# Kernel optimization log

Hardware: AMD Instinct MI355X
Metric: run time of the kernel (lower is better)

The kernel has to match this reference:

```python
import jax, jax.numpy as jnp
import numpy as np

B, C, H, W = 4, 192, 256, 256
P = 8          # patch_size; d_model = P, input_size = P*P
R = 4          # FFN expansion ratio
SLOPE = 0.01   # torch default leaky_relu negative_slope


def _conv(x, w, pad):
    return jax.lax.conv_general_dilated(x, w, (1, 1), pad,
                                        dimension_numbers=('NCHW', 'OIHW', 'NCHW'))


def setup_inputs() -> dict:
    key = jax.random.key(0)
    ks = jax.random.split(key, 16)
    p2 = P * P
    s = 0.05
    return {
        'x':  jax.random.normal(ks[0], (B, C, H, W), jnp.float32),
        # per-window linear attention params (torch Linear stored as (in,out))
        'Wq': jax.random.normal(ks[1], (p2, P), jnp.float32) * s,
        'bq': jnp.zeros((P,), jnp.float32),
        'Wk': jax.random.normal(ks[2], (p2, P), jnp.float32) * s,
        'bk': jnp.zeros((P,), jnp.float32),
        'Wv': jax.random.normal(ks[3], (p2, P), jnp.float32) * s,
        'bv': jnp.zeros((P,), jnp.float32),
        'Wo': jax.random.normal(ks[4], (P, p2), jnp.float32) * s,
        'bo': jnp.zeros((p2,), jnp.float32),
        # FFN conv params
        'W1': jax.random.normal(ks[5], (C * R, C, 1, 1), jnp.float32) * s,
        'b1': jnp.zeros((C * R,), jnp.float32),
        'W2': jax.random.normal(ks[6], (C * R, C * R, 3, 3), jnp.float32) * s,
        'b2': jnp.zeros((C * R,), jnp.float32),
        'W3': jax.random.normal(ks[7], (C, C * R, 1, 1), jnp.float32) * s,
        'b3': jnp.zeros((C,), jnp.float32),
    }


def reference(x, Wq, bq, Wk, bk, Wv, bv, Wo, bo, W1, b1, W2, b2, W3, b3):
    Bb, Cc, Hh, Ww = x.shape
    nh, nw = Hh // P, Ww // P
    N = nh * nw
    # crop patches: (B, N, C, P*P), window-major row order (i over rows, j over cols)
    xp = (x.reshape(Bb, Cc, nh, P, nw, P)
           .transpose(0, 2, 4, 1, 3, 5)
           .reshape(Bb, N, Cc, P * P))
    # softplus-kernel linear attention over the CHANNEL axis (weight is CxC per window)
    q = jax.nn.softplus(xp @ Wq + bq)            # (B,N,C,P)
    k = jax.nn.softplus(xp @ Wk + bk)            # (B,N,C,P)
    v = xp @ Wv + bv                              # (B,N,C,P)
    w = jnp.einsum('bncd,bnhd->bnch', q, k)      # (B,N,C,C)
    r = jnp.einsum('bnch,bnhd->bncd', w, v)      # (B,N,C,P)
    attn = r @ Wo + bo                            # (B,N,C,P*P)
    y = xp + attn                                 # in-place residual in the original
    # Merge_patches: cat along height then reshape == contiguous reinterpret
    feat = (y.reshape(Bb, N, Cc, P, P)
             .transpose(0, 2, 1, 3, 4)
             .reshape(Bb, Cc, nh * P, nw * P))
    h = jax.nn.leaky_relu(_conv(feat, W1, 'VALID') + b1[:, None, None], SLOPE)
    h = jax.nn.leaky_relu(_conv(h, W2, 'SAME') + b2[:, None, None], SLOPE)
    out = jax.nn.leaky_relu(_conv(h, W3, 'VALID') + b3[:, None, None], SLOPE)
    return out
```

## Files before the change

kernel.cpp:

```cpp
#include <hip/hip_runtime.h>
#include <stdint.h>
#include <math.h>

typedef _Float16 half_t;
typedef _Float16 f16x8 __attribute__((ext_vector_type(8)));
typedef float f32x4 __attribute__((ext_vector_type(4)));

#define SLOPE 0.01f

__device__ inline float leaky(float v) { return v > 0.f ? v : SLOPE * v; }

__device__ inline void stage16(const half_t* g, half_t* l) {
    __builtin_amdgcn_global_load_lds(
        (const __attribute__((address_space(1))) unsigned int*)g,
        (__attribute__((address_space(3))) unsigned int*)l, 16, 0, 0);
}

__device__ inline float softplusf(float v) {
    return v > 20.f ? v : log1pf(expf(v));
}

__global__ void prep_kernel(const float* __restrict__ W1, const float* __restrict__ W2,
                            const float* __restrict__ W3,
                            half_t* __restrict__ B1w, half_t* __restrict__ B2w,
                            half_t* __restrict__ B3w)
{
    const unsigned idx = blockIdx.x * 256u + threadIdx.x;
    const unsigned n2 = 768u * 6912u;
    if (idx < n2) {
        unsigned oc = idx / 6912u;
        unsigned rem = idx - oc * 6912u;
        unsigned tap = rem / 768u;
        unsigned ic = rem - tap * 768u;
        unsigned ky = tap / 3u, kx = tap - ky * 3u;
        B2w[idx] = (half_t)W2[(((size_t)oc * 768u + ic) * 3u + ky) * 3u + kx];
    } else if (idx < n2 + 147456u) {
        unsigned i = idx - n2;
        B1w[i] = (half_t)W1[i];
    } else if (idx < n2 + 294912u) {
        unsigned i = idx - n2 - 147456u;
        B3w[i] = (half_t)W3[i];
    }
}

__global__ __launch_bounds__(256, 2)
void attn_kernel(const float* __restrict__ x,
                 const float* __restrict__ Wq, const float* __restrict__ bq,
                 const float* __restrict__ Wk, const float* __restrict__ bk,
                 const float* __restrict__ Wv, const float* __restrict__ bv,
                 const float* __restrict__ Wo, const float* __restrict__ bo,
                 half_t* __restrict__ featN)
{
    __shared__ half_t xls[192 * 65];
    __shared__ float wqL[512], wkL[512], wvL[512], woL[512];
    __shared__ float bqL[8], bkL[8], bvL[8], boL[64];
    __shared__ float kls[192 * 9], vls[192 * 9];
    __shared__ float sls[64];

    const int t = threadIdx.x;
    const int blk = blockIdx.x;
    const int b = blk >> 10;
    const int n = blk & 1023;
    const int wi = n >> 5, wj = n & 31;

    for (int i = t; i < 512; i += 256) {
        wqL[i] = Wq[i]; wkL[i] = Wk[i]; wvL[i] = Wv[i]; woL[i] = Wo[i];
    }
    if (t < 8)  { bqL[t] = bq[t]; bkL[t] = bk[t]; bvL[t] = bv[t]; }
    if (t < 64) boL[t] = bo[t];

    #pragma unroll
    for (int i = 0; i < 6; ++i) {
        int idx = t + i * 256;
        int c = idx >> 3, py = idx & 7;
        const float* src = x + (((size_t)b * 192 + c) * 256 + (wi * 8 + py)) * 256 + wj * 8;
        float4 v0 = *(const float4*)src;
        float4 v1 = *(const float4*)(src + 4);
        half_t* dst = &xls[c * 65 + py * 8];
        dst[0] = (half_t)v0.x; dst[1] = (half_t)v0.y; dst[2] = (half_t)v0.z; dst[3] = (half_t)v0.w;
        dst[4] = (half_t)v1.x; dst[5] = (half_t)v1.y; dst[6] = (half_t)v1.z; dst[7] = (half_t)v1.w;
    }
    __syncthreads();

    float qf[8], kf[8], vf[8];
    if (t < 192) {
        #pragma unroll
        for (int d = 0; d < 8; ++d) { qf[d] = bqL[d]; kf[d] = bkL[d]; vf[d] = bvL[d]; }
        const half_t* xr = &xls[t * 65];
        for (int p = 0; p < 64; ++p) {
            float xv = (float)xr[p];
            const float* wqp = &wqL[p * 8];
            const float* wkp = &wkL[p * 8];
            const float* wvp = &wvL[p * 8];
            #pragma unroll
            for (int d = 0; d < 8; ++d) {
                qf[d] += xv * wqp[d];
                kf[d] += xv * wkp[d];
                vf[d] += xv * wvp[d];
            }
        }
        #pragma unroll
        for (int d = 0; d < 8; ++d) {
            qf[d] = softplusf(qf[d]);
            kf[d] = softplusf(kf[d]);
            kls[t * 9 + d] = kf[d];
            vls[t * 9 + d] = vf[d];
        }
    }
    __syncthreads();
    if (t < 64) {
        int e = t >> 3, dd = t & 7;
        float s = 0.f;
        for (int c = 0; c < 192; ++c) s += kls[c * 9 + e] * vls[c * 9 + dd];
        sls[t] = s;
    }
    __syncthreads();
    if (t < 192) {
        float rf[8];
        #pragma unroll
        for (int d = 0; d < 8; ++d) {
            float s = 0.f;
            #pragma unroll
            for (int e = 0; e < 8; ++e) s += qf[e] * sls[e * 8 + d];
            rf[d] = s;
        }
        half_t* xr = &xls[t * 65];
        for (int p = 0; p < 64; ++p) {
            float a = boL[p];
            #pragma unroll
            for (int d = 0; d < 8; ++d) a += rf[d] * woL[d * 64 + p];
            xr[p] = (half_t)((float)xr[p] + a);
        }
    }
    __syncthreads();
    half_t* dst = featN + ((size_t)b * 65536 + (size_t)n * 64) * 192;
    for (int i = 0; i < 48; ++i) {
        int idx = t + i * 256;
        int p = idx / 192, c = idx - p * 192;
        dst[idx] = xls[c * 65 + p];
    }
}

__global__ __launch_bounds__(256, 2)
void conv1_kernel(const half_t* __restrict__ featN, const half_t* __restrict__ B1w,
                  const float* __restrict__ b1, half_t* __restrict__ h1p, int batch)
{
    __shared__ half_t As[128 * 64];
    __shared__ half_t Bs[128 * 64];
    const int t = threadIdx.x;
    const int lane = t & 63;
    const int w = t >> 6;
    const int m0 = blockIdx.x * 128;
    const int n0 = blockIdx.y * 128;
    const int wm = (w >> 1) * 64, wn = (w & 1) * 64;
    const int rbase = t >> 3;
    const int g = (t & 7) ^ (rbase & 7);
    const int ar = lane & 15, kc = lane >> 4;

    f32x4 acc[4][4];
    #pragma unroll
    for (int i = 0; i < 4; ++i)
        #pragma unroll
        for (int j = 0; j < 4; ++j) acc[i][j] = (f32x4){0.f, 0.f, 0.f, 0.f};

    const size_t mb = (size_t)batch * 65536 + m0;

    for (int s = 0; s < 3; ++s) {
        const int k0 = s * 64;
        const half_t* ga = featN + (mb + rbase) * 192 + k0 + g * 8;
        const half_t* gb = B1w + (size_t)(n0 + rbase) * 192 + k0 + g * 8;
        half_t* la = As + t * 8;
        half_t* lb = Bs + t * 8;
        #pragma unroll
        for (int i = 0; i < 4; ++i) {
            stage16(ga + (size_t)32 * i * 192, la + 2048 * i);
            stage16(gb + (size_t)32 * i * 192, lb + 2048 * i);
        }
        __syncthreads();
        #pragma unroll
        for (int kh = 0; kh < 2; ++kh) {
            f16x8 af[4], bfr[4];
            const int c = kh * 4 + kc;
            #pragma unroll
            for (int mf = 0; mf < 4; ++mf) {
                int r = wm + mf * 16 + ar;
                af[mf] = *(const f16x8*)&As[(r * 8 + (c ^ (r & 7))) * 8];
            }
            #pragma unroll
            for (int nf = 0; nf < 4; ++nf) {
                int r = wn + nf * 16 + ar;
                bfr[nf] = *(const f16x8*)&Bs[(r * 8 + (c ^ (r & 7))) * 8];
            }
            #pragma unroll
            for (int mf = 0; mf < 4; ++mf)
                #pragma unroll
                for (int nf = 0; nf < 4; ++nf)
                    acc[mf][nf] = __builtin_amdgcn_mfma_f32_16x16x32_f16(af[mf], bfr[nf], acc[mf][nf], 0, 0, 0);
        }
        __syncthreads();
    }

    const int y = m0 >> 8, x0 = m0 & 255;
    half_t* outrow = h1p + ((size_t)(y + 1) * 258 + (x0 + 1)) * 768;
    #pragma unroll
    for (int nf = 0; nf < 4; ++nf) {
        int n = n0 + wn + nf * 16 + ar;
        float bias = b1[n];
        #pragma unroll
        for (int mf = 0; mf < 4; ++mf) {
            #pragma unroll
            for (int r4 = 0; r4 < 4; ++r4) {
                int local = wm + mf * 16 + kc * 4 + r4;
                outrow[(size_t)local * 768 + n] = (half_t)leaky(acc[mf][nf][r4] + bias);
            }
        }
    }
}

__device__ __forceinline__ void c2_stage_A(half_t* As, int buf, int h,
    const half_t* __restrict__ h1p, int y, int kstep, int t, int cg)
{
    const int tap = kstep / 12, icc = kstep - tap * 12;
    const int ky = tap / 3, kx = tap - ky * 3;
    const int row0 = t >> 3;
    const half_t* g = h1p + ((size_t)(y + ky) * 258 + (kx + h * 128 + row0)) * 768
                      + icc * 64 + cg;
    half_t* l = As + (buf * 2 + h) * 8192 + t * 8;
    stage16(g, l);
    stage16(g + (size_t)64 * 768, l + 4096);
}

__device__ __forceinline__ void c2_stage_B(half_t* Bs, int buf, int h,
    const half_t* __restrict__ B2w, int n0, int kstep, int t, int cg)
{
    const int tap = kstep / 12, icc = kstep - tap * 12;
    const int row0 = t >> 3;
    const half_t* g = B2w + (size_t)(n0 + h * 128 + row0) * 6912
                      + tap * 768 + icc * 64 + cg;
    half_t* l = Bs + (buf * 2 + h) * 8192 + t * 8;
    stage16(g, l);
    stage16(g + (size_t)64 * 6912, l + 4096);
}

#define SBAR __builtin_amdgcn_s_barrier()
#define SB0  __builtin_amdgcn_sched_barrier(0)
#define LGKM(N) asm volatile("s_waitcnt lgkmcnt(" #N ")" ::: "memory")
#define VMC(N)  asm volatile("s_waitcnt vmcnt(" #N ")" ::: "memory")

#define RDA(MQ, BUF)                                                             \
  _Pragma("unroll")                                                              \
  for (int mf = 0; mf < 4; ++mf)                                                 \
    _Pragma("unroll")                                                            \
    for (int kh = 0; kh < 2; ++kh) {                                             \
      const int lr = wm * 64 + mf * 16 + ar;                                     \
      const int ch = (kh * 4 + kc) ^ (lr & 7);                                   \
      af[MQ][mf][kh] = *(const f16x8*)&As[((BUF)*2 + (MQ))*8192 + lr*64 + ch*8]; \
    }

#define RDB(NQ, BUF)                                                             \
  _Pragma("unroll")                                                              \
  for (int nf = 0; nf < 2; ++nf)                                                 \
    _Pragma("unroll")                                                            \
    for (int kh = 0; kh < 2; ++kh) {                                             \
      const int lc = wn * 32 + nf * 16 + ar;                                     \
      const int ch = (kh * 4 + kc) ^ (lc & 7);                                   \
      bf[NQ][nf][kh] = *(const f16x8*)&Bs[((BUF)*2 + (NQ))*8192 + lc*64 + ch*8]; \
    }

#define MMA16(MQ, NQ)                                                            \
  {                                                                              \
    __builtin_amdgcn_s_setprio(1);                                               \
    _Pragma("unroll")                                                            \
    for (int kh = 0; kh < 2; ++kh)                                               \
      _Pragma("unroll")                                                          \
      for (int mf = 0; mf < 4; ++mf)                                             \
        _Pragma("unroll")                                                        \
        for (int nf = 0; nf < 2; ++nf)                                           \
          acc[(MQ)*2+(NQ)][mf][nf] = __builtin_amdgcn_mfma_f32_16x16x32_f16(     \
              af[MQ][mf][kh], bf[NQ][nf][kh], acc[(MQ)*2+(NQ)][mf][nf], 0, 0, 0);\
    __builtin_amdgcn_s_setprio(0);                                               \
  }

__global__ __launch_bounds__(512, 2)
void conv2_kernel(const half_t* __restrict__ h1p, const half_t* __restrict__ B2w,
                  const float* __restrict__ b2, half_t* __restrict__ h2)
{
    __shared__ half_t As[4 * 8192];
    __shared__ half_t Bs[4 * 8192];

    const int t = threadIdx.x;
    const int lane = t & 63;
    const int w = t >> 6;
    const int wm = w >> 2, wn = w & 3;
    const int ar = lane & 15, kc = lane >> 4;
    const int cg = (((t & 7) ^ ((t >> 3) & 7)) << 3);

    const int bid = blockIdx.x;
    const int xcd = bid & 7, sid = bid >> 3;
    const int wg = xcd * 96 + sid;
    const int mtile = wg / 3;
    const int nt = wg - mtile * 3;
    const int y = mtile;
    const int m0 = mtile * 256;
    const int n0 = nt * 256;

    f32x4 acc[4][4][2];
    #pragma unroll
    for (int q = 0; q < 4; ++q)
        #pragma unroll
        for (int i = 0; i < 4; ++i)
            #pragma unroll
            for (int j = 0; j < 2; ++j) acc[q][i][j] = (f32x4){0.f, 0.f, 0.f, 0.f};

    f16x8 af[2][4][2];
    f16x8 bf[2][2][2];

    c2_stage_A(As, 0, 0, h1p, y, 0, t, cg);
    c2_stage_A(As, 0, 1, h1p, y, 0, t, cg);
    c2_stage_B(Bs, 0, 0, B2w, n0, 0, t, cg);
    c2_stage_B(Bs, 0, 1, B2w, n0, 0, t, cg);
    c2_stage_A(As, 1, 0, h1p, y, 1, t, cg);
    c2_stage_A(As, 1, 1, h1p, y, 1, t, cg);
    c2_stage_B(Bs, 1, 0, B2w, n0, 1, t, cg);
    c2_stage_B(Bs, 1, 1, B2w, n0, 1, t, cg);
    VMC(0);
    SBAR; SB0;
    RDB(0, 0); SB0;
    RDA(0, 0);

    for (int i = 0; i < 53; ++i) {
        const int k2 = 2 * i + 2;
        const int k3 = 2 * i + 3;
        RDB(1, 0); SB0;
        RDA(1, 0);
        LGKM(12); SB0;
        MMA16(0, 0);
        SBAR;
        c2_stage_A(As, 0, 0, h1p, y, k2, t, cg);
        c2_stage_B(Bs, 0, 0, B2w, n0, k2, t, cg);
        LGKM(8); SB0;
        MMA16(0, 1);
        SBAR;
        LGKM(0); SB0;
        MMA16(1, 1);
        SBAR;
        c2_stage_A(As, 0, 1, h1p, y, k2, t, cg);
        c2_stage_B(Bs, 0, 1, B2w, n0, k2, t, cg);
        VMC(8);
        SBAR; SB0;
        MMA16(1, 0);
        SB0;
        RDB(0, 1); SB0;
        RDA(0, 1);
        SBAR;
        RDB(1, 1); SB0;
        RDA(1, 1);
        LGKM(12); SB0;
        MMA16(0, 0);
        SBAR;
        c2_stage_A(As, 1, 0, h1p, y, k3, t, cg);
        c2_stage_B(Bs, 1, 0, B2w, n0, k3, t, cg);
        LGKM(8); SB0;
        MMA16(0, 1);
        SBAR;
        LGKM(0); SB0;
        MMA16(1, 1);
        SBAR;
        c2_stage_A(As, 1, 1, h1p, y, k3, t, cg);
        c2_stage_B(Bs, 1, 1, B2w, n0, k3, t, cg);
        VMC(8);
        SBAR; SB0;
        MMA16(1, 0);
        SB0;
        RDB(0, 0); SB0;
        RDA(0, 0);
        SBAR;
    }
    {
        RDB(1, 0); SB0;
        RDA(1, 0);
        LGKM(12); SB0;
        MMA16(0, 0);
        SBAR;
        LGKM(8); SB0;
        MMA16(0, 1);
        SBAR;
        LGKM(0); SB0;
        MMA16(1, 1);
        SBAR;
        VMC(0);
        SBAR; SB0;
        MMA16(1, 0);
        SB0;
        RDB(0, 1); SB0;
        RDA(0, 1);
        SBAR;
        RDB(1, 1); SB0;
        RDA(1, 1);
        LGKM(12); SB0;
        MMA16(0, 0);
        SBAR;
        LGKM(8); SB0;
        MMA16(0, 1);
        SBAR;
        LGKM(0); SB0;
        MMA16(1, 1);
        SBAR;
        MMA16(1, 0);
    }

    #pragma unroll
    for (int q = 0; q < 4; ++q) {
        const int mq = q >> 1, nq = q & 1;
        #pragma unroll
        for (int nf = 0; nf < 2; ++nf) {
            const int col = n0 + nq * 128 + wn * 32 + nf * 16 + ar;
            const float bias = b2[col];
            #pragma unroll
            for (int mf = 0; mf < 4; ++mf) {
                const int row = m0 + mq * 128 + wm * 64 + mf * 16 + kc * 4;
                half_t* op = h2 + (size_t)row * 768 + col;
                #pragma unroll
                for (int r4 = 0; r4 < 4; ++r4)
                    op[(size_t)r4 * 768] = (half_t)leaky(acc[q][mf][nf][r4] + bias);
            }
        }
    }
}

__global__ __launch_bounds__(256, 2)
void conv3_kernel(const half_t* __restrict__ h2, const half_t* __restrict__ B3w,
                  const float* __restrict__ b3, float* __restrict__ out, int batch)
{
    __shared__ half_t As[128 * 64];
    __shared__ half_t Bs[192 * 64];
    const int t = threadIdx.x;
    const int lane = t & 63;
    const int w = t >> 6;
    const int m0 = blockIdx.x * 128;
    const int wm = (w >> 1) * 64;
    const int wn = (w & 1) * 96;
    const int rbase = t >> 3;
    const int g = (t & 7) ^ (rbase & 7);
    const int ar = lane & 15, kc = lane >> 4;

    f32x4 acc[4][6];
    #pragma unroll
    for (int i = 0; i < 4; ++i)
        #pragma unroll
        for (int j = 0; j < 6; ++j) acc[i][j] = (f32x4){0.f, 0.f, 0.f, 0.f};

    for (int s = 0; s < 12; ++s) {
        const int k0 = s * 64;
        const half_t* ga = h2 + (size_t)(m0 + rbase) * 768 + k0 + g * 8;
        const half_t* gb = B3w + (size_t)rbase * 768 + k0 + g * 8;
        half_t* la = As + t * 8;
        half_t* lb = Bs + t * 8;
        #pragma unroll
        for (int i = 0; i < 4; ++i) stage16(ga + (size_t)32 * i * 768, la + 2048 * i);
        #pragma unroll
        for (int i = 0; i < 6; ++i) stage16(gb + (size_t)32 * i * 768, lb + 2048 * i);
        __syncthreads();
        #pragma unroll
        for (int kh = 0; kh < 2; ++kh) {
            f16x8 af[4], bfr[6];
            const int c = kh * 4 + kc;
            #pragma unroll
            for (int mf = 0; mf < 4; ++mf) {
                int r = wm + mf * 16 + ar;
                af[mf] = *(const f16x8*)&As[(r * 8 + (c ^ (r & 7))) * 8];
            }
            #pragma unroll
            for (int nf = 0; nf < 6; ++nf) {
                int r = wn + nf * 16 + ar;
                bfr[nf] = *(const f16x8*)&Bs[(r * 8 + (c ^ (r & 7))) * 8];
            }
            #pragma unroll
            for (int mf = 0; mf < 4; ++mf)
                #pragma unroll
                for (int nf = 0; nf < 6; ++nf)
                    acc[mf][nf] = __builtin_amdgcn_mfma_f32_16x16x32_f16(af[mf], bfr[nf], acc[mf][nf], 0, 0, 0);
        }
        __syncthreads();
    }

    #pragma unroll
    for (int nf = 0; nf < 6; ++nf) {
        int n = wn + nf * 16 + ar;
        float bias = b3[n];
        float* op = out + ((size_t)batch * 192 + n) * 65536 + m0;
        #pragma unroll
        for (int mf = 0; mf < 4; ++mf) {
            int local = wm + mf * 16 + kc * 4;
            f32x4 v;
            #pragma unroll
            for (int r4 = 0; r4 < 4; ++r4) v[r4] = leaky(acc[mf][nf][r4] + bias);
            *(f32x4*)(op + local) = v;
        }
    }
}

extern "C" void kernel_launch(void* const* d_in, const int* in_sizes, int n_in,
                              void* d_out, int out_size, void* d_ws, size_t ws_size,
                              hipStream_t stream)
{
    const float* x  = (const float*)d_in[0];
    const float* Wq = (const float*)d_in[1];
    const float* bq = (const float*)d_in[2];
    const float* Wk = (const float*)d_in[3];
    const float* bk = (const float*)d_in[4];
    const float* Wv = (const float*)d_in[5];
    const float* bv = (const float*)d_in[6];
    const float* Wo = (const float*)d_in[7];
    const float* bo = (const float*)d_in[8];
    const float* W1 = (const float*)d_in[9];
    const float* b1 = (const float*)d_in[10];
    const float* W2 = (const float*)d_in[11];
    const float* b2 = (const float*)d_in[12];
    const float* W3 = (const float*)d_in[13];
    const float* b3 = (const float*)d_in[14];

    char* ws = (char*)d_ws;
    const size_t OFF_B1   = 0;
    const size_t OFF_B3   = 294912;
    const size_t OFF_B2   = 589824;
    const size_t OFF_FEAT = 11206656;
    const size_t OFF_H1P  = 111869952;
    const size_t OFF_H2   = 214124544;
    const size_t WS_NEED  = 314787840;
    if (ws_size < WS_NEED) return;

    half_t* B1w   = (half_t*)(ws + OFF_B1);
    half_t* B3w   = (half_t*)(ws + OFF_B3);
    half_t* B2w   = (half_t*)(ws + OFF_B2);
    half_t* featN = (half_t*)(ws + OFF_FEAT);
    half_t* h1p   = (half_t*)(ws + OFF_H1P);
    half_t* h2    = (half_t*)(ws + OFF_H2);

    hipMemsetAsync(h1p, 0, 102254592, stream);
    prep_kernel<<<21888, 256, 0, stream>>>(W1, W2, W3, B1w, B2w, B3w);
    attn_kernel<<<4096, 256, 0, stream>>>(x, Wq, bq, Wk, bk, Wv, bv, Wo, bo, featN);

    for (int b = 0; b < 4; ++b) {
        conv1_kernel<<<dim3(512, 6), 256, 0, stream>>>(featN, B1w, b1, h1p, b);
        conv2_kernel<<<768, 512, 0, stream>>>(h1p, B2w, b2, h2);
        conv3_kernel<<<dim3(512, 1), 256, 0, stream>>>(h2, B3w, b3, (float*)d_out, b);
    }
}
```

Baseline: 2.907 ms.

## Rebalance conv2 GEMM LDS-read pipeline with ping-pong B fragments and new tile mapping

The main loop of the 3x3 conv GEMM is rescheduled. B fragments now go into separate ping-pong register sets (bf0A/bf0B/bf1), so the next k-step's B0 reads and A reads can be issued before the last MMA of the current step, and one barrier per half-step is removed. The workgroup-to-tile mapping also changes so each XCD handles a contiguous run of M tiles for each N tile, which alters L2 reuse of A rows. The prologue waits only for the first stage (VMC(8)) instead of all loads. This raises register pressure and depends on tricky waitcnt and barrier ordering for correctness.

```diff
diff --git a/kernel.cpp b/kernel.cpp
--- a/kernel.cpp
+++ b/kernel.cpp
@@ -257,17 +257,17 @@
       af[MQ][mf][kh] = *(const f16x8*)&As[((BUF)*2 + (MQ))*8192 + lr*64 + ch*8]; \
     }
 
-#define RDB(NQ, BUF)                                                             \
+#define RDBX(REG, NQ, BUF)                                                       \
   _Pragma("unroll")                                                              \
   for (int nf = 0; nf < 2; ++nf)                                                 \
     _Pragma("unroll")                                                            \
     for (int kh = 0; kh < 2; ++kh) {                                             \
       const int lc = wn * 32 + nf * 16 + ar;                                     \
       const int ch = (kh * 4 + kc) ^ (lc & 7);                                   \
-      bf[NQ][nf][kh] = *(const f16x8*)&Bs[((BUF)*2 + (NQ))*8192 + lc*64 + ch*8]; \
-    }
-
-#define MMA16(MQ, NQ)                                                            \
+      REG[nf][kh] = *(const f16x8*)&Bs[((BUF)*2 + (NQ))*8192 + lc*64 + ch*8];    \
+    }
+
+#define MMA16X(MQ, NQ, BREG)                                                     \
   {                                                                              \
     __builtin_amdgcn_s_setprio(1);                                               \
     _Pragma("unroll")                                                            \
@@ -277,7 +277,7 @@
         _Pragma("unroll")                                                        \
         for (int nf = 0; nf < 2; ++nf)                                           \
           acc[(MQ)*2+(NQ)][mf][nf] = __builtin_amdgcn_mfma_f32_16x16x32_f16(     \
-              af[MQ][mf][kh], bf[NQ][nf][kh], acc[(MQ)*2+(NQ)][mf][nf], 0, 0, 0);\
+              af[MQ][mf][kh], BREG[nf][kh], acc[(MQ)*2+(NQ)][mf][nf], 0, 0, 0);  \
     __builtin_amdgcn_s_setprio(0);                                               \
   }
 
@@ -297,9 +297,8 @@
 
     const int bid = blockIdx.x;
     const int xcd = bid & 7, sid = bid >> 3;
-    const int wg = xcd * 96 + sid;
-    const int mtile = wg / 3;
-    const int nt = wg - mtile * 3;
+    const int nt = sid >> 5;
+    const int mtile = xcd * 32 + (sid & 31);
     const int y = mtile;
     const int m0 = mtile * 256;
     const int n0 = nt * 256;
@@ -313,7 +312,9 @@
             for (int j = 0; j < 2; ++j) acc[q][i][j] = (f32x4){0.f, 0.f, 0.f, 0.f};
 
     f16x8 af[2][4][2];
-    f16x8 bf[2][2][2];
+    f16x8 bf1[2][2];
+    f16x8 bf0A[2][2];
+    f16x8 bf0B[2][2];
 
     c2_stage_A(As, 0, 0, h1p, y, 0, t, cg);
     c2_stage_A(As, 0, 1, h1p, y, 0, t, cg);
@@ -323,90 +324,84 @@
     c2_stage_A(As, 1, 1, h1p, y, 1, t, cg);
     c2_stage_B(Bs, 1, 0, B2w, n0, 1, t, cg);
     c2_stage_B(Bs, 1, 1, B2w, n0, 1, t, cg);
-    VMC(0);
+    VMC(8);
     SBAR; SB0;
-    RDB(0, 0); SB0;
+    RDBX(bf0A, 0, 0); SB0;
     RDA(0, 0);
 
     for (int i = 0; i < 53; ++i) {
         const int k2 = 2 * i + 2;
         const int k3 = 2 * i + 3;
-        RDB(1, 0); SB0;
-        RDA(1, 0);
-        LGKM(12); SB0;
-        MMA16(0, 0);
+        RDBX(bf1, 1, 0);
+        LGKM(4); SB0;
+        MMA16X(0, 0, bf0A);
         SBAR;
         c2_stage_A(As, 0, 0, h1p, y, k2, t, cg);
         c2_stage_B(Bs, 0, 0, B2w, n0, k2, t, cg);
+        RDA(1, 0);
         LGKM(8); SB0;
-        MMA16(0, 1);
+        MMA16X(0, 1, bf1);
         SBAR;
         LGKM(0); SB0;
-        MMA16(1, 1);
+        MMA16X(1, 1, bf1);
         SBAR;
         c2_stage_A(As, 0, 1, h1p, y, k2, t, cg);
         c2_stage_B(Bs, 0, 1, B2w, n0, k2, t, cg);
         VMC(8);
         SBAR; SB0;
-        MMA16(1, 0);
-        SB0;
-        RDB(0, 1); SB0;
         RDA(0, 1);
-        SBAR;
-        RDB(1, 1); SB0;
-        RDA(1, 1);
-        LGKM(12); SB0;
-        MMA16(0, 0);
+        RDBX(bf0B, 0, 1); SB0;
+        MMA16X(1, 0, bf0A);
+        RDBX(bf1, 1, 1);
+        LGKM(4); SB0;
+        MMA16X(0, 0, bf0B);
         SBAR;
         c2_stage_A(As, 1, 0, h1p, y, k3, t, cg);
         c2_stage_B(Bs, 1, 0, B2w, n0, k3, t, cg);
+        RDA(1, 1);
         LGKM(8); SB0;
-        MMA16(0, 1);
+        MMA16X(0, 1, bf1);
         SBAR;
         LGKM(0); SB0;
-        MMA16(1, 1);
+        MMA16X(1, 1, bf1);
         SBAR;
         c2_stage_A(As, 1, 1, h1p, y, k3, t, cg);
         c2_stage_B(Bs, 1, 1, B2w, n0, k3, t, cg);
         VMC(8);
         SBAR; SB0;
-        MMA16(1, 0);
-        SB0;
-        RDB(0, 0); SB0;
         RDA(0, 0);
-        SBAR;
+        RDBX(bf0A, 0, 0); SB0;
+        MMA16X(1, 0, bf0B);
     }
     {
-        RDB(1, 0); SB0;
+        RDBX(bf1, 1, 0);
+        LGKM(4); SB0;
+        MMA16X(0, 0, bf0A);
+        SBAR;
         RDA(1, 0);
-        LGKM(12); SB0;
-        MMA16(0, 0);
-        SBAR;
         LGKM(8); SB0;
-        MMA16(0, 1);
+        MMA16X(0, 1, bf1);
         SBAR;
         LGKM(0); SB0;
-        MMA16(1, 1);
+        MMA16X(1, 1, bf1);
         SBAR;
         VMC(0);
         SBAR; SB0;
-        MMA16(1, 0);
-        SB0;
-        RDB(0, 1); SB0;
         RDA(0, 1);
-        SBAR;
-        RDB(1, 1); SB0;
+        RDBX(bf0B, 0, 1); SB0;
+        MMA16X(1, 0, bf0A);
+        RDBX(bf1, 1, 1);
+        LGKM(4); SB0;
+        MMA16X(0, 0, bf0B);
+        SBAR;
         RDA(1, 1);
-        LGKM(12); SB0;
-        MMA16(0, 0);
-        SBAR;
         LGKM(8); SB0;
-        MMA16(0, 1);
+        MMA16X(0, 1, bf1);
         SBAR;
         LGKM(0); SB0;
-        MMA16(1, 1);
-        SBAR;
-        MMA16(1, 0);
+        MMA16X(1, 1, bf1);
+        SBAR;
+        MMA16X(1, 0, bf0B);
     }
 
     #pragma unroll
```

Measured after the change: 3.409 ms. 1.17x slower.
